# Kernel optimization log

Measured on AMD Instinct MI355X. Metric: run time of the kernel, lower is better.

The kernel has to match this reference:

```python
import jax, jax.numpy as jnp
import numpy as np

B, C, H, W = 8, 512, 32, 32
NUM_HEADS = 8
HEAD_DIM = C // NUM_HEADS


def setup_inputs() -> dict:
    key = jax.random.key(0)
    k1, k2, k3 = jax.random.split(key, 3)
    s = 0.02
    return {
        "x": jax.random.normal(k1, (B, C, H, W), dtype=jnp.float32),
        "W_qkv": jax.random.normal(k2, (3 * C, C), dtype=jnp.float32) * s,
        "b_qkv": jnp.zeros((3 * C,), dtype=jnp.float32),
        "W_proj": jax.random.normal(k3, (C, C), dtype=jnp.float32) * s,
        "b_proj": jnp.zeros((C,), dtype=jnp.float32),
    }


def reference(x, W_qkv, b_qkv, W_proj, b_proj):
    b, c, h, w = x.shape
    n = h * w  # seq_len in raster order
    nh, hd = NUM_HEADS, c // NUM_HEADS
    scale = hd ** -0.5

    # b c h w -> b n c
    x_seq = x.reshape(b, c, n).transpose(0, 2, 1)
    qkv = x_seq @ W_qkv.T + b_qkv  # (b, n, 3c)
    # b n (3 nh hd) -> 3, b, nh, n, hd
    qkv = qkv.reshape(b, n, 3, nh, hd).transpose(2, 0, 3, 1, 4)
    q, k, v = qkv[0], qkv[1], qkv[2]

    attn = jnp.einsum('bhnd,bhmd->bhnm', q, k) * scale
    causal = jnp.tril(jnp.ones((n, n), dtype=bool))
    attn = jnp.where(causal, attn, -jnp.inf)
    attn = jax.nn.softmax(attn, axis=-1)

    out = jnp.einsum('bhnm,bhmd->bhnd', attn, v)
    out = out.transpose(0, 2, 1, 3).reshape(b, n, c)  # b n c
    out = out @ W_proj.T + b_proj
    # b (h w) c -> b c h w
    return out.transpose(0, 2, 1).reshape(b, c, h, w)
```

## Files before the change

### kernel.cpp

```cpp
#include <hip/hip_runtime.h>
#include <hip/hip_bf16.h>
#include <math.h>

#define B_  8
#define C_  512
#define N_  1024
#define NH_ 8
#define HD_ 64
#define C3_ 1536

typedef __bf16 bf16x8 __attribute__((ext_vector_type(8)));
typedef float  f32x4  __attribute__((ext_vector_type(4)));
typedef __hip_bfloat16 bf16;

__device__ __forceinline__ f32x4 mfma16(const bf16x8& a, const bf16x8& b, const f32x4& c) {
    return __builtin_amdgcn_mfma_f32_16x16x32_bf16(a, b, c, 0, 0, 0);
}

__device__ __forceinline__ void ld_lds16(const bf16* g, bf16* l_uniform) {
    __builtin_amdgcn_global_load_lds(
        (const __attribute__((address_space(1))) void*)(uintptr_t)g,
        (__attribute__((address_space(3))) void*)(uintptr_t)l_uniform,
        16, 0, 0);
}


__global__ __launch_bounds__(256) void cvt_bf16(const float* __restrict__ in,
                                                bf16* __restrict__ out, int n) {
    int i = blockIdx.x * 256 + threadIdx.x;
    if (i < n) out[i] = __float2bfloat16(in[i]);
}

__global__ __launch_bounds__(256) void transpose_x(const float* __restrict__ x,
                                                   bf16* __restrict__ xb) {
    __shared__ float T[32][33];
    const int n0 = blockIdx.x * 32, c0 = blockIdx.y * 32, b = blockIdx.z;
    const int tx = threadIdx.x, ty = threadIdx.y;
    const float* xp = x + ((size_t)b * C_ + c0) * N_ + n0;
#pragma unroll
    for (int l = 0; l < 4; ++l)
        T[ty + 8 * l][tx] = xp[(ty + 8 * l) * N_ + tx];
    __syncthreads();
    bf16* xo = xb + ((size_t)b * N_ + n0) * C_ + c0;
#pragma unroll
    for (int l = 0; l < 4; ++l)
        xo[(ty + 8 * l) * C_ + tx] = __float2bfloat16(T[tx][ty + 8 * l]);
}

__global__ __launch_bounds__(256) void qkv_mfma(const bf16* __restrict__ xb,
                                                const bf16* __restrict__ Wqb,
                                                const float* __restrict__ bq,
                                                bf16* __restrict__ Qb,
                                                bf16* __restrict__ Kb,
                                                bf16* __restrict__ Vt) {
    __shared__ bf16 As[128 * 32];
    __shared__ bf16 Bs[128 * 32];
    __shared__ bf16 Vl[4][16][20];
    const int tid = threadIdx.x, w = tid >> 6, lane = tid & 63;
    const int lo = lane & 15, hi = lane >> 4;
    const int j0 = blockIdx.x * 128;
    const int m0 = blockIdx.y * 128;
    const int b  = m0 >> 10;

    const int srow = w * 32 + (lane >> 2);
    const int scol = (lane & 3) * 8;
    const bf16* gA = xb  + (size_t)(m0 + srow) * C_ + scol;
    const bf16* gB = Wqb + (size_t)(j0 + srow) * C_ + scol;
    bf16* lA = As + (w * 32) * 32;
    bf16* lB = Bs + (w * 32) * 32;

    f32x4 acc[4][4];
#pragma unroll
    for (int mt = 0; mt < 4; ++mt)
#pragma unroll
        for (int jt = 0; jt < 4; ++jt)
            acc[mt][jt] = (f32x4){0.f, 0.f, 0.f, 0.f};

    for (int k0 = 0; k0 < C_; k0 += 32) {
        ld_lds16(gA + k0, lA);
        ld_lds16(gA + (size_t)16 * C_ + k0, lA + 16 * 32);
        ld_lds16(gB + k0, lB);
        ld_lds16(gB + (size_t)16 * C_ + k0, lB + 16 * 32);
        __syncthreads();

        bf16x8 af[4], bfr[4];
#pragma unroll
        for (int mt = 0; mt < 4; ++mt)
            af[mt] = *(const bf16x8*)(As + ((w & 1) * 64 + mt * 16 + lo) * 32 + hi * 8);
#pragma unroll
        for (int jt = 0; jt < 4; ++jt)
            bfr[jt] = *(const bf16x8*)(Bs + ((w >> 1) * 64 + jt * 16 + lo) * 32 + hi * 8);
#pragma unroll
        for (int mt = 0; mt < 4; ++mt)
#pragma unroll
            for (int jt = 0; jt < 4; ++jt)
                acc[mt][jt] = mfma16(af[mt], bfr[jt], acc[mt][jt]);
        __syncthreads();
    }

    const int mb = (w & 1) * 64, jb = (w >> 1) * 64;
    const int nbase = (m0 & 1023) + mb;
#pragma unroll
    for (int jt = 0; jt < 4; ++jt) {
        const int j16 = j0 + jb + jt * 16;
        const float bias = bq[j16 + lo];
        if (j16 < 512) {
            const int h = j16 >> 6, d = (j16 & 63) + lo;
            bf16* qp = Qb + ((size_t)(b * NH_ + h) * N_) * HD_ + d;
#pragma unroll
            for (int mt = 0; mt < 4; ++mt)
#pragma unroll
                for (int r = 0; r < 4; ++r) {
                    int n = nbase + mt * 16 + hi * 4 + r;
                    qp[(size_t)n * HD_] = __float2bfloat16((acc[mt][jt][r] + bias) * 0.125f);
                }
        } else if (j16 < 1024) {
            const int jj = j16 - 512;
            const int h = jj >> 6, d = (jj & 63) + lo;
            bf16* kp = Kb + ((size_t)(b * NH_ + h) * N_) * HD_ + d;
#pragma unroll
            for (int mt = 0; mt < 4; ++mt)
#pragma unroll
                for (int r = 0; r < 4; ++r) {
                    int n = nbase + mt * 16 + hi * 4 + r;
                    kp[(size_t)n * HD_] = __float2bfloat16(acc[mt][jt][r] + bias);
                }
        } else {
            const int jj = j16 - 1024;
            const int h = jj >> 6, dbase = jj & 63;
            bf16* vp = Vt + ((size_t)(b * NH_ + h) * HD_ + dbase) * N_ + nbase;
#pragma unroll
            for (int mt = 0; mt < 4; ++mt) {
#pragma unroll
                for (int r = 0; r < 4; ++r)
                    Vl[w][hi * 4 + r][lo] = __float2bfloat16(acc[mt][jt][r] + bias);
#pragma unroll
                for (int r = 0; r < 4; ++r)
                    vp[(size_t)(hi * 4 + r) * N_ + mt * 16 + lo] = Vl[w][lo][hi * 4 + r];
            }
        }
    }
}

__device__ __forceinline__ void attn_chain(
    const bf16x8& q0, const bf16x8& q1,
    const bf16x8& k00, const bf16x8& k01, const bf16x8& k10, const bf16x8& k11,
    const bf16x8& v0, const bf16x8& v1, const bf16x8& v2, const bf16x8& v3,
    int qw, int key0, int lo, int hi,
    bf16 (*pl)[40], f32x4* O, float* Lp)
{
    f32x4 S0 = {0.f, 0.f, 0.f, 0.f};
    f32x4 S1 = {0.f, 0.f, 0.f, 0.f};
    S0 = mfma16(q0, k00, S0);
    S0 = mfma16(q1, k01, S0);
    S1 = mfma16(q0, k10, S1);
    S1 = mfma16(q1, k11, S1);

    if (key0 + 31 > qw) {
#pragma unroll
        for (int r = 0; r < 4; ++r) {
            int q = qw + hi * 4 + r;
            if (key0 + lo > q)      S0[r] = -1e30f;
            if (key0 + 16 + lo > q) S1[r] = -1e30f;
        }
    }

#pragma unroll
    for (int r = 0; r < 4; ++r) {
        float p0 = __expf(S0[r]);
        float p1 = __expf(S1[r]);
        Lp[r] += p0 + p1;
        pl[hi * 4 + r][lo]      = __float2bfloat16(p0);
        pl[hi * 4 + r][16 + lo] = __float2bfloat16(p1);
    }

    bf16x8 pa = *(const bf16x8*)(&pl[lo][hi * 8]);
    O[0] = mfma16(pa, v0, O[0]);
    O[1] = mfma16(pa, v1, O[1]);
    O[2] = mfma16(pa, v2, O[2]);
    O[3] = mfma16(pa, v3, O[3]);
}

__device__ __forceinline__ void attn_store(bf16* __restrict__ ao, int b, int h, int qw,
                                           int lo, int hi, f32x4* O, float* Lp)
{
    float rL[4];
#pragma unroll
    for (int r = 0; r < 4; ++r) {
        float Ls = Lp[r];
#pragma unroll
        for (int off = 1; off < 16; off <<= 1)
            Ls += __shfl_xor(Ls, off, 64);
        rL[r] = 1.f / Ls;
    }
#pragma unroll
    for (int t = 0; t < 4; ++t)
#pragma unroll
        for (int r = 0; r < 4; ++r) {
            int q = qw + hi * 4 + r;
            ao[((size_t)b * N_ + q) * C_ + h * HD_ + t * 16 + lo] =
                __float2bfloat16(O[t][r] * rL[r]);
        }
}

__global__ __launch_bounds__(256) void attn_mfma(const bf16* __restrict__ Qb,
                                                 const bf16* __restrict__ Kb,
                                                 const bf16* __restrict__ Vt,
                                                 bf16* __restrict__ ao) {
    __shared__ __align__(16) bf16 Pl[4][2][16][40];
    const int wv   = threadIdx.x >> 6;
    const int lane = threadIdx.x & 63;
    const int lo   = lane & 15;
    const int hi   = lane >> 4;
    const int bh   = blockIdx.x & 63;
    const int pi   = (blockIdx.x >> 6) * 4 + wv;
    const int qwA  = pi * 16;
    const int qwB  = (63 - pi) * 16;

    const bf16* Qh = Qb + (size_t)bh * N_ * HD_;
    const bf16* Kh = Kb + (size_t)bh * N_ * HD_;
    const bf16* Vh = Vt + (size_t)bh * HD_ * N_;

    const bf16x8 qA0 = *(const bf16x8*)(Qh + (qwA + lo) * HD_ + hi * 8);
    const bf16x8 qA1 = *(const bf16x8*)(Qh + (qwA + lo) * HD_ + 32 + hi * 8);
    const bf16x8 qB0 = *(const bf16x8*)(Qh + (qwB + lo) * HD_ + hi * 8);
    const bf16x8 qB1 = *(const bf16x8*)(Qh + (qwB + lo) * HD_ + 32 + hi * 8);

    f32x4 OA[4], OB[4];
    float LA[4], LB[4];
#pragma unroll
    for (int r = 0; r < 4; ++r) {
        OA[0][r] = OA[1][r] = OA[2][r] = OA[3][r] = 0.f;
        OB[0][r] = OB[1][r] = OB[2][r] = OB[3][r] = 0.f;
        LA[r] = 0.f; LB[r] = 0.f;
    }

    const int nkbA = (qwA + 47) >> 5;
    const int nkbB = (qwB + 47) >> 5;

    for (int kb = 0; kb < nkbB; ++kb) {
        const int key0 = kb * 32;
        const bf16* kp = Kh + (size_t)(key0 + lo) * HD_ + hi * 8;
        bf16x8 k00 = *(const bf16x8*)(kp);
        bf16x8 k01 = *(const bf16x8*)(kp + 32);
        bf16x8 k10 = *(const bf16x8*)(kp + 16 * HD_);
        bf16x8 k11 = *(const bf16x8*)(kp + 16 * HD_ + 32);
        const bf16* vp = Vh + (size_t)lo * N_ + key0 + hi * 8;
        bf16x8 v0 = *(const bf16x8*)(vp);
        bf16x8 v1 = *(const bf16x8*)(vp + 16 * N_);
        bf16x8 v2 = *(const bf16x8*)(vp + 32 * N_);
        bf16x8 v3 = *(const bf16x8*)(vp + 48 * N_);

        attn_chain(qB0, qB1, k00, k01, k10, k11, v0, v1, v2, v3,
                   qwB, key0, lo, hi, Pl[wv][1], OB, LB);
        if (kb < nkbA)
            attn_chain(qA0, qA1, k00, k01, k10, k11, v0, v1, v2, v3,
                       qwA, key0, lo, hi, Pl[wv][0], OA, LA);
    }

    const int b = bh >> 3, h = bh & 7;
    attn_store(ao, b, h, qwA, lo, hi, OA, LA);
    attn_store(ao, b, h, qwB, lo, hi, OB, LB);
}

__global__ __launch_bounds__(256) void proj_mfma(const bf16* __restrict__ aob,
                                                 const bf16* __restrict__ Wpb,
                                                 const float* __restrict__ bp,
                                                 float* __restrict__ out) {
    __shared__ bf16 As[64 * 32];
    __shared__ bf16 Bs[128 * 32];
    const int tid = threadIdx.x, w = tid >> 6, lane = tid & 63;
    const int lo = lane & 15, hi = lane >> 4;
    const int j0 = blockIdx.x * 64;
    const int n0 = blockIdx.y * 128;
    const int b  = n0 >> 10;

    const int r4 = lane >> 2, c8 = (lane & 3) * 8;
    const bf16* gA = Wpb + (size_t)(j0 + w * 16 + r4) * C_ + c8;
    const bf16* gB = aob + (size_t)(n0 + w * 32 + r4) * C_ + c8;
    bf16* lA = As + (w * 16) * 32;
    bf16* lB = Bs + (w * 32) * 32;

    f32x4 acc[2][4];
#pragma unroll
    for (int mt = 0; mt < 2; ++mt)
#pragma unroll
        for (int jt = 0; jt < 4; ++jt)
            acc[mt][jt] = (f32x4){0.f, 0.f, 0.f, 0.f};

    for (int k0 = 0; k0 < C_; k0 += 32) {
        ld_lds16(gA + k0, lA);
        ld_lds16(gB + k0, lB);
        ld_lds16(gB + (size_t)16 * C_ + k0, lB + 16 * 32);
        __syncthreads();

        bf16x8 af[2], bfr[4];
#pragma unroll
        for (int mt = 0; mt < 2; ++mt)
            af[mt] = *(const bf16x8*)(As + ((w & 1) * 32 + mt * 16 + lo) * 32 + hi * 8);
#pragma unroll
        for (int jt = 0; jt < 4; ++jt)
            bfr[jt] = *(const bf16x8*)(Bs + ((w >> 1) * 64 + jt * 16 + lo) * 32 + hi * 8);
#pragma unroll
        for (int mt = 0; mt < 2; ++mt)
#pragma unroll
            for (int jt = 0; jt < 4; ++jt)
                acc[mt][jt] = mfma16(af[mt], bfr[jt], acc[mt][jt]);
        __syncthreads();
    }

#pragma unroll
    for (int mt = 0; mt < 2; ++mt)
#pragma unroll
        for (int r = 0; r < 4; ++r) {
            const int j = j0 + (w & 1) * 32 + mt * 16 + hi * 4 + r;
            const float bias = bp[j];
            float* op = out + ((size_t)(b * C_ + j)) * N_ + (n0 & 1023) + (w >> 1) * 64 + lo;
#pragma unroll
            for (int jt = 0; jt < 4; ++jt)
                op[jt * 16] = acc[mt][jt][r] + bias;
        }
}

extern "C" void kernel_launch(void* const* d_in, const int* in_sizes, int n_in,
                              void* d_out, int out_size, void* d_ws, size_t ws_size,
                              hipStream_t stream) {
    const float* x  = (const float*)d_in[0];
    const float* Wq = (const float*)d_in[1];
    const float* bq = (const float*)d_in[2];
    const float* Wp = (const float*)d_in[3];
    const float* bp = (const float*)d_in[4];
    float* out = (float*)d_out;

    const size_t headElems = (size_t)B_ * NH_ * N_ * HD_;
    bf16* xb  = (bf16*)d_ws;
    bf16* Wqb = xb + (size_t)B_ * N_ * C_;
    bf16* Wpb = Wqb + (size_t)C3_ * C_;
    bf16* Qb  = Wpb + (size_t)C_ * C_;
    bf16* Kb  = Qb + headElems;
    bf16* Vt  = Kb + headElems;
    bf16* aob = Vt + headElems;

    cvt_bf16<<<dim3((C3_ * C_ + 255) / 256), dim3(256), 0, stream>>>(Wq, Wqb, C3_ * C_);
    cvt_bf16<<<dim3((C_ * C_ + 255) / 256), dim3(256), 0, stream>>>(Wp, Wpb, C_ * C_);
    transpose_x<<<dim3(N_ / 32, C_ / 32, B_), dim3(32, 8), 0, stream>>>(x, xb);

    qkv_mfma<<<dim3(C3_ / 128, (B_ * N_) / 128), dim3(256), 0, stream>>>(xb, Wqb, bq, Qb, Kb, Vt);
    attn_mfma<<<dim3(8 * 64), dim3(256), 0, stream>>>(Qb, Kb, Vt, aob);
    proj_mfma<<<dim3(C_ / 64, (B_ * N_) / 128), dim3(256), 0, stream>>>(aob, Wpb, bp, out);
}
```

Before: 170.2 us.

## Split attention key loop across wave pairs and merge partials in LDS

Each query-pair is now handled by two waves that take alternate key blocks, which doubles the grid to 1024 blocks. The partial O and L accumulators are exchanged through shared memory and combined before normalisation. This works without a max rescale because the softmax carries no running max. It also merges the two weight-conversion launches into one kernel. The aim is more parallelism and shorter per-wave serial chains in attention, at the cost of extra LDS use and a block-wide sync.

New measurement: 174.7 us. +2.6%, slower.

```diff
diff --git a/kernel.cpp b/kernel.cpp
--- a/kernel.cpp
+++ b/kernel.cpp
@@ -25,10 +25,16 @@
 }
 
 
-__global__ __launch_bounds__(256) void cvt_bf16(const float* __restrict__ in,
-                                                bf16* __restrict__ out, int n) {
+__global__ __launch_bounds__(256) void cvt_w(const float* __restrict__ Wq,
+                                             const float* __restrict__ Wp,
+                                             bf16* __restrict__ Wqb,
+                                             bf16* __restrict__ Wpb) {
     int i = blockIdx.x * 256 + threadIdx.x;
-    if (i < n) out[i] = __float2bfloat16(in[i]);
+    if (i < C3_ * C_) Wqb[i] = __float2bfloat16(Wq[i]);
+    else {
+        int j = i - C3_ * C_;
+        if (j < C_ * C_) Wpb[j] = __float2bfloat16(Wp[j]);
+    }
 }
 
 __global__ __launch_bounds__(256) void transpose_x(const float* __restrict__ x,
@@ -98,8 +104,8 @@
         __syncthreads();
     }
 
-    const int mb = (w & 1) * 64, jb = (w >> 1) * 64;
-    const int nbase = (m0 & 1023) + mb;
+    const int jb = (w >> 1) * 64;
+    const int nbase = (m0 & 1023) + (w & 1) * 64;
 #pragma unroll
     for (int jt = 0; jt < 4; ++jt) {
         const int j16 = j0 + jb + jt * 16;
@@ -181,39 +187,23 @@
     O[3] = mfma16(pa, v3, O[3]);
 }
 
-__device__ __forceinline__ void attn_store(bf16* __restrict__ ao, int b, int h, int qw,
-                                           int lo, int hi, f32x4* O, float* Lp)
-{
-    float rL[4];
-#pragma unroll
-    for (int r = 0; r < 4; ++r) {
-        float Ls = Lp[r];
-#pragma unroll
-        for (int off = 1; off < 16; off <<= 1)
-            Ls += __shfl_xor(Ls, off, 64);
-        rL[r] = 1.f / Ls;
-    }
-#pragma unroll
-    for (int t = 0; t < 4; ++t)
-#pragma unroll
-        for (int r = 0; r < 4; ++r) {
-            int q = qw + hi * 4 + r;
-            ao[((size_t)b * N_ + q) * C_ + h * HD_ + t * 16 + lo] =
-                __float2bfloat16(O[t][r] * rL[r]);
-        }
-}
-
 __global__ __launch_bounds__(256) void attn_mfma(const bf16* __restrict__ Qb,
                                                  const bf16* __restrict__ Kb,
                                                  const bf16* __restrict__ Vt,
                                                  bf16* __restrict__ ao) {
     __shared__ __align__(16) bf16 Pl[4][2][16][40];
+    __shared__ float Oc[2][2][16][68];
+    __shared__ float Lc[2][2][4][64];
+
     const int wv   = threadIdx.x >> 6;
     const int lane = threadIdx.x & 63;
     const int lo   = lane & 15;
     const int hi   = lane >> 4;
     const int bh   = blockIdx.x & 63;
-    const int pi   = (blockIdx.x >> 6) * 4 + wv;
+    const int blk  = blockIdx.x >> 6;
+    const int pl_  = wv >> 1;
+    const int ks   = wv & 1;
+    const int pi   = blk * 2 + pl_;
     const int qwA  = pi * 16;
     const int qwB  = (63 - pi) * 16;
 
@@ -238,7 +228,7 @@
     const int nkbA = (qwA + 47) >> 5;
     const int nkbB = (qwB + 47) >> 5;
 
-    for (int kb = 0; kb < nkbB; ++kb) {
+    for (int kb = ks; kb < nkbB; kb += 2) {
         const int key0 = kb * 32;
         const bf16* kp = Kh + (size_t)(key0 + lo) * HD_ + hi * 8;
         bf16x8 k00 = *(const bf16x8*)(kp);
@@ -258,9 +248,45 @@
                        qwA, key0, lo, hi, Pl[wv][0], OA, LA);
     }
 
+    {
+        const int ch = 1 - ks;
+        f32x4* Od = (ks == 0) ? OB : OA;
+        float* Ld  = (ks == 0) ? LB : LA;
+#pragma unroll
+        for (int t = 0; t < 4; ++t)
+#pragma unroll
+            for (int r = 0; r < 4; ++r)
+                Oc[pl_][ch][hi * 4 + r][t * 16 + lo] = Od[t][r];
+#pragma unroll
+        for (int r = 0; r < 4; ++r)
+            Lc[pl_][ch][r][lane] = Ld[r];
+    }
+    __syncthreads();
+
     const int b = bh >> 3, h = bh & 7;
-    attn_store(ao, b, h, qwA, lo, hi, OA, LA);
-    attn_store(ao, b, h, qwB, lo, hi, OB, LB);
+    const int ch = ks;
+    const int qw = (ks == 0) ? qwA : qwB;
+    f32x4* Om = (ks == 0) ? OA : OB;
+    float* Lm  = (ks == 0) ? LA : LB;
+
+    float rL[4];
+#pragma unroll
+    for (int r = 0; r < 4; ++r) {
+        float Ls = Lm[r] + Lc[pl_][ch][r][lane];
+#pragma unroll
+        for (int off = 1; off < 16; off <<= 1)
+            Ls += __shfl_xor(Ls, off, 64);
+        rL[r] = 1.f / Ls;
+    }
+#pragma unroll
+    for (int t = 0; t < 4; ++t)
+#pragma unroll
+        for (int r = 0; r < 4; ++r) {
+            int q = qw + hi * 4 + r;
+            float o = Om[t][r] + Oc[pl_][ch][hi * 4 + r][t * 16 + lo];
+            ao[((size_t)b * N_ + q) * C_ + h * HD_ + t * 16 + lo] =
+                __float2bfloat16(o * rL[r]);
+        }
 }
 
 __global__ __launch_bounds__(256) void proj_mfma(const bf16* __restrict__ aob,
@@ -341,11 +367,10 @@
     bf16* Vt  = Kb + headElems;
     bf16* aob = Vt + headElems;
 
-    cvt_bf16<<<dim3((C3_ * C_ + 255) / 256), dim3(256), 0, stream>>>(Wq, Wqb, C3_ * C_);
-    cvt_bf16<<<dim3((C_ * C_ + 255) / 256), dim3(256), 0, stream>>>(Wp, Wpb, C_ * C_);
+    cvt_w<<<dim3((C3_ * C_ + C_ * C_ + 255) / 256), dim3(256), 0, stream>>>(Wq, Wp, Wqb, Wpb);
     transpose_x<<<dim3(N_ / 32, C_ / 32, B_), dim3(32, 8), 0, stream>>>(x, xb);
 
     qkv_mfma<<<dim3(C3_ / 128, (B_ * N_) / 128), dim3(256), 0, stream>>>(xb, Wqb, bq, Qb, Kb, Vt);
-    attn_mfma<<<dim3(8 * 64), dim3(256), 0, stream>>>(Qb, Kb, Vt, aob);
+    attn_mfma<<<dim3(16 * 64), dim3(256), 0, stream>>>(Qb, Kb, Vt, aob);
     proj_mfma<<<dim3(C_ / 64, (B_ * N_) / 128), dim3(256), 0, stream>>>(aob, Wpb, bp, out);
 }
```

## Give each attention wave one query tile and merge weight conversions

Applied to the files above, without the earlier changes.

The attention kernel stops pairing a short and a long query tile per wave, which shared K/V loads between them. Each wave now handles a single 16-row query tile, and the grid doubles to 1024 blocks. Within a block the four waves take tiles g, g+16, g+32 and g+48, which spreads causal work unevenly across waves. The two weight-conversion kernels are also fused into one launch to cut launch overhead. In exchange, K/V loads are no longer reused across two query tiles, and per-wave load imbalance grows.

Result: slower. 182.3 us (+7.1%).

```diff
diff --git a/kernel.cpp b/kernel.cpp
--- a/kernel.cpp
+++ b/kernel.cpp
@@ -25,10 +25,16 @@
 }
 
 
-__global__ __launch_bounds__(256) void cvt_bf16(const float* __restrict__ in,
-                                                bf16* __restrict__ out, int n) {
+__global__ __launch_bounds__(256) void cvt_w(const float* __restrict__ Wq,
+                                             const float* __restrict__ Wp,
+                                             bf16* __restrict__ Wqb,
+                                             bf16* __restrict__ Wpb) {
     int i = blockIdx.x * 256 + threadIdx.x;
-    if (i < n) out[i] = __float2bfloat16(in[i]);
+    if (i < C3_ * C_) Wqb[i] = __float2bfloat16(Wq[i]);
+    else {
+        int j = i - C3_ * C_;
+        if (j < C_ * C_) Wpb[j] = __float2bfloat16(Wp[j]);
+    }
 }
 
 __global__ __launch_bounds__(256) void transpose_x(const float* __restrict__ x,
@@ -98,8 +104,8 @@
         __syncthreads();
     }
 
-    const int mb = (w & 1) * 64, jb = (w >> 1) * 64;
-    const int nbase = (m0 & 1023) + mb;
+    const int jb = (w >> 1) * 64;
+    const int nbase = (m0 & 1023) + (w & 1) * 64;
 #pragma unroll
     for (int jt = 0; jt < 4; ++jt) {
         const int j16 = j0 + jb + jt * 16;
@@ -141,6 +147,7 @@
         }
     }
 }
+
 
 __device__ __forceinline__ void attn_chain(
     const bf16x8& q0, const bf16x8& q1,
@@ -181,64 +188,37 @@
     O[3] = mfma16(pa, v3, O[3]);
 }
 
-__device__ __forceinline__ void attn_store(bf16* __restrict__ ao, int b, int h, int qw,
-                                           int lo, int hi, f32x4* O, float* Lp)
-{
-    float rL[4];
-#pragma unroll
-    for (int r = 0; r < 4; ++r) {
-        float Ls = Lp[r];
-#pragma unroll
-        for (int off = 1; off < 16; off <<= 1)
-            Ls += __shfl_xor(Ls, off, 64);
-        rL[r] = 1.f / Ls;
-    }
-#pragma unroll
-    for (int t = 0; t < 4; ++t)
-#pragma unroll
-        for (int r = 0; r < 4; ++r) {
-            int q = qw + hi * 4 + r;
-            ao[((size_t)b * N_ + q) * C_ + h * HD_ + t * 16 + lo] =
-                __float2bfloat16(O[t][r] * rL[r]);
-        }
-}
-
 __global__ __launch_bounds__(256) void attn_mfma(const bf16* __restrict__ Qb,
                                                  const bf16* __restrict__ Kb,
                                                  const bf16* __restrict__ Vt,
                                                  bf16* __restrict__ ao) {
-    __shared__ __align__(16) bf16 Pl[4][2][16][40];
+    __shared__ __align__(16) bf16 Pl[4][16][40];
     const int wv   = threadIdx.x >> 6;
     const int lane = threadIdx.x & 63;
     const int lo   = lane & 15;
     const int hi   = lane >> 4;
     const int bh   = blockIdx.x & 63;
-    const int pi   = (blockIdx.x >> 6) * 4 + wv;
-    const int qwA  = pi * 16;
-    const int qwB  = (63 - pi) * 16;
+    const int g    = blockIdx.x >> 6;
+    const int qt   = g + 16 * wv;
+    const int qw   = qt * 16;
 
     const bf16* Qh = Qb + (size_t)bh * N_ * HD_;
     const bf16* Kh = Kb + (size_t)bh * N_ * HD_;
     const bf16* Vh = Vt + (size_t)bh * HD_ * N_;
 
-    const bf16x8 qA0 = *(const bf16x8*)(Qh + (qwA + lo) * HD_ + hi * 8);
-    const bf16x8 qA1 = *(const bf16x8*)(Qh + (qwA + lo) * HD_ + 32 + hi * 8);
-    const bf16x8 qB0 = *(const bf16x8*)(Qh + (qwB + lo) * HD_ + hi * 8);
-    const bf16x8 qB1 = *(const bf16x8*)(Qh + (qwB + lo) * HD_ + 32 + hi * 8);
-
-    f32x4 OA[4], OB[4];
-    float LA[4], LB[4];
+    const bf16x8 q0 = *(const bf16x8*)(Qh + (qw + lo) * HD_ + hi * 8);
+    const bf16x8 q1 = *(const bf16x8*)(Qh + (qw + lo) * HD_ + 32 + hi * 8);
+
+    f32x4 O[4];
+    float Lp[4];
 #pragma unroll
     for (int r = 0; r < 4; ++r) {
-        OA[0][r] = OA[1][r] = OA[2][r] = OA[3][r] = 0.f;
-        OB[0][r] = OB[1][r] = OB[2][r] = OB[3][r] = 0.f;
-        LA[r] = 0.f; LB[r] = 0.f;
-    }
-
-    const int nkbA = (qwA + 47) >> 5;
-    const int nkbB = (qwB + 47) >> 5;
-
-    for (int kb = 0; kb < nkbB; ++kb) {
+        O[0][r] = O[1][r] = O[2][r] = O[3][r] = 0.f;
+        Lp[r] = 0.f;
+    }
+
+    const int nkb = (qw + 47) >> 5;
+    for (int kb = 0; kb < nkb; ++kb) {
         const int key0 = kb * 32;
         const bf16* kp = Kh + (size_t)(key0 + lo) * HD_ + hi * 8;
         bf16x8 k00 = *(const bf16x8*)(kp);
@@ -251,16 +231,28 @@
         bf16x8 v2 = *(const bf16x8*)(vp + 32 * N_);
         bf16x8 v3 = *(const bf16x8*)(vp + 48 * N_);
 
-        attn_chain(qB0, qB1, k00, k01, k10, k11, v0, v1, v2, v3,
-                   qwB, key0, lo, hi, Pl[wv][1], OB, LB);
-        if (kb < nkbA)
-            attn_chain(qA0, qA1, k00, k01, k10, k11, v0, v1, v2, v3,
-                       qwA, key0, lo, hi, Pl[wv][0], OA, LA);
+        attn_chain(q0, q1, k00, k01, k10, k11, v0, v1, v2, v3,
+                   qw, key0, lo, hi, Pl[wv], O, Lp);
     }
 
     const int b = bh >> 3, h = bh & 7;
-    attn_store(ao, b, h, qwA, lo, hi, OA, LA);
-    attn_store(ao, b, h, qwB, lo, hi, OB, LB);
+    float rL[4];
+#pragma unroll
+    for (int r = 0; r < 4; ++r) {
+        float Ls = Lp[r];
+#pragma unroll
+        for (int off = 1; off < 16; off <<= 1)
+            Ls += __shfl_xor(Ls, off, 64);
+        rL[r] = 1.f / Ls;
+    }
+#pragma unroll
+    for (int t = 0; t < 4; ++t)
+#pragma unroll
+        for (int r = 0; r < 4; ++r) {
+            int q = qw + hi * 4 + r;
+            ao[((size_t)b * N_ + q) * C_ + h * HD_ + t * 16 + lo] =
+                __float2bfloat16(O[t][r] * rL[r]);
+        }
 }
 
 __global__ __launch_bounds__(256) void proj_mfma(const bf16* __restrict__ aob,
@@ -341,11 +333,10 @@
     bf16* Vt  = Kb + headElems;
     bf16* aob = Vt + headElems;
 
-    cvt_bf16<<<dim3((C3_ * C_ + 255) / 256), dim3(256), 0, stream>>>(Wq, Wqb, C3_ * C_);
-    cvt_bf16<<<dim3((C_ * C_ + 255) / 256), dim3(256), 0, stream>>>(Wp, Wpb, C_ * C_);
+    cvt_w<<<dim3((C3_ * C_ + C_ * C_ + 255) / 256), dim3(256), 0, stream>>>(Wq, Wp, Wqb, Wpb);
     transpose_x<<<dim3(N_ / 32, C_ / 32, B_), dim3(32, 8), 0, stream>>>(x, xb);
 
     qkv_mfma<<<dim3(C3_ / 128, (B_ * N_) / 128), dim3(256), 0, stream>>>(xb, Wqb, bq, Qb, Kb, Vt);
-    attn_mfma<<<dim3(8 * 64), dim3(256), 0, stream>>>(Qb, Kb, Vt, aob);
+    attn_mfma<<<dim3(16 * 64), dim3(256), 0, stream>>>(Qb, Kb, Vt, aob);
     proj_mfma<<<dim3(C_ / 64, (B_ * N_) / 128), dim3(256), 0, stream>>>(aob, Wpb, bp, out);
 }
```
